# Optimization experiments

Hardware: AMD Instinct MI355X
Metric: run time of the kernel (lower is better)

## Reference

```python
import jax, jax.numpy as jnp
import numpy as np

N_NODES = 10000
N_EDGES = 160000
N_GRAPHS = 64
X_IN = 128
HID = 64
EDGE_DIM = 16
HEADS = 4
# (in_dim, out_dim_per_head) for the 3 TransformerConv layers (concat=False)
DIMS = [(X_IN, HID), (HID, 2 * HID), (2 * HID, HID)]
WNAMES = [f"{n}{l}" for l in (1, 2, 3) for n in ("wq", "bq", "wk", "bk", "wv", "bv", "we", "ws", "bs")]


def setup_inputs() -> dict:
    key = jax.random.key(0)
    ks = iter(jax.random.split(key, 64))
    inp = {}
    inp["x"] = jax.random.normal(next(ks), (N_NODES, X_IN), jnp.float32)
    inp["edge_index"] = jax.random.randint(next(ks), (2, N_EDGES), 0, N_NODES)
    inp["edge_attr"] = jax.random.normal(next(ks), (N_EDGES, EDGE_DIM), jnp.float32)
    inp["batch"] = jnp.sort(jax.random.randint(next(ks), (N_NODES,), 0, N_GRAPHS))
    for l, (din, dout) in enumerate(DIMS, 1):
        hd = HEADS * dout
        for nm, shape in [("wq", (din, hd)), ("wk", (din, hd)), ("wv", (din, hd)),
                          ("we", (EDGE_DIM, hd)), ("ws", (din, dout))]:
            inp[f"{nm}{l}"] = jax.random.normal(next(ks), shape, jnp.float32) * 0.05
        inp[f"bq{l}"] = jnp.zeros((hd,), jnp.float32)
        inp[f"bk{l}"] = jnp.zeros((hd,), jnp.float32)
        inp[f"bv{l}"] = jnp.zeros((hd,), jnp.float32)
        inp[f"bs{l}"] = jnp.zeros((dout,), jnp.float32)
    return inp


def _transformer_conv(x, src, dst, edge_attr, wq, bq, wk, bk, wv, bv, we, ws, bs, dout):
    """PyG TransformerConv, concat=False, root_weight=True, with edge features."""
    N = x.shape[0]
    q = (x @ wq + bq).reshape(N, HEADS, dout)
    k = (x @ wk + bk).reshape(N, HEADS, dout)
    v = (x @ wv + bv).reshape(N, HEADS, dout)
    e = (edge_attr @ we).reshape(-1, HEADS, dout)  # [E, H, C]
    k_j = k[src] + e                               # edge-conditioned keys
    alpha = jnp.einsum("ehd,ehd->eh", q[dst], k_j) * (1.0 / float(dout) ** 0.5)  # [E, H]
    # numerically stable segment softmax over incoming edges of each dst node
    a_max = jax.ops.segment_max(alpha, dst, num_segments=N)
    ex = jnp.exp(alpha - a_max[dst])
    den = jax.ops.segment_sum(ex, dst, num_segments=N)
    attn = ex / den[dst]
    agg = jax.ops.segment_sum((v[src] + e) * attn[..., None], dst, num_segments=N)  # [N, H, C]
    return agg.mean(axis=1) + x @ ws + bs  # concat=False -> head mean; + skip


def _forward(x, edge_attr, edge_index, batch, params):
    src, dst = edge_index[0], edge_index[1]
    h = x
    for l, (_, dout) in enumerate(DIMS, 1):
        p = [params[f"{n}{l}"] for n in ("wq", "bq", "wk", "bk", "wv", "bv", "we", "ws", "bs")]
        h = jax.nn.elu(_transformer_conv(h, src, dst, edge_attr, *p, dout))
    # global mean pool over graphs
    s = jax.ops.segment_sum(h, batch, num_segments=N_GRAPHS)
    cnt = jax.ops.segment_sum(jnp.ones((h.shape[0], 1), h.dtype), batch, num_segments=N_GRAPHS)
    return s / jnp.maximum(cnt, 1.0)


def reference(x, edge_index, edge_attr, batch,
              wq1, bq1, wk1, bk1, wv1, bv1, we1, ws1, bs1,
              wq2, bq2, wk2, bk2, wv2, bv2, we2, ws2, bs2,
              wq3, bq3, wk3, bk3, wv3, bv3, we3, ws3, bs3):
    params = dict(locals())
    return _forward(x, edge_attr, edge_index, batch, params)
```

## Files before the change

kernel.cpp:

```cpp
#include <hip/hip_runtime.h>
#include <hip/hip_fp16.h>
#include <math.h>

#define N_NODES 10000
#define N_EDGES 160000
#define N_GRAPHS 64

using half8 = __attribute__((ext_vector_type(8))) _Float16;
using floatx4 = __attribute__((ext_vector_type(4))) float;
using h2v = __attribute__((ext_vector_type(2))) _Float16;

template <int NV> struct KW;
template <> struct KW<1> { using T = uint2; };
template <> struct KW<2> { using T = uint4; };

__device__ inline void cvt_kv(const uint2& w, float4* dst) {
  float2 a = __half22float2(*reinterpret_cast<const __half2*>(&w.x));
  float2 b = __half22float2(*reinterpret_cast<const __half2*>(&w.y));
  dst[0] = make_float4(a.x, a.y, b.x, b.y);
}
__device__ inline void cvt_kv(const uint4& w, float4* dst) {
  float2 a = __half22float2(*reinterpret_cast<const __half2*>(&w.x));
  float2 b = __half22float2(*reinterpret_cast<const __half2*>(&w.y));
  float2 c = __half22float2(*reinterpret_cast<const __half2*>(&w.z));
  float2 d = __half22float2(*reinterpret_cast<const __half2*>(&w.w));
  dst[0] = make_float4(a.x, a.y, b.x, b.y);
  dst[1] = make_float4(c.x, c.y, d.x, d.y);
}

#if __has_builtin(__builtin_amdgcn_fdot2)
__device__ inline float dot_qk(const uint2& k, const uint2& q, float c) {
  c = __builtin_amdgcn_fdot2(__builtin_bit_cast(h2v, k.x), __builtin_bit_cast(h2v, q.x), c, false);
  c = __builtin_amdgcn_fdot2(__builtin_bit_cast(h2v, k.y), __builtin_bit_cast(h2v, q.y), c, false);
  return c;
}
__device__ inline float dot_qk(const uint4& k, const uint4& q, float c) {
  c = __builtin_amdgcn_fdot2(__builtin_bit_cast(h2v, k.x), __builtin_bit_cast(h2v, q.x), c, false);
  c = __builtin_amdgcn_fdot2(__builtin_bit_cast(h2v, k.y), __builtin_bit_cast(h2v, q.y), c, false);
  c = __builtin_amdgcn_fdot2(__builtin_bit_cast(h2v, k.z), __builtin_bit_cast(h2v, q.z), c, false);
  c = __builtin_amdgcn_fdot2(__builtin_bit_cast(h2v, k.w), __builtin_bit_cast(h2v, q.w), c, false);
  return c;
}
#else
__device__ inline float dot_qk(const uint2& k, const uint2& q, float c) {
  float4 kk[1], qq[1];
  cvt_kv(k, kk); cvt_kv(q, qq);
  return c + qq[0].x * kk[0].x + qq[0].y * kk[0].y + qq[0].z * kk[0].z + qq[0].w * kk[0].w;
}
__device__ inline float dot_qk(const uint4& k, const uint4& q, float c) {
  float4 kk[2], qq[2];
  cvt_kv(k, kk); cvt_kv(q, qq);
  c += qq[0].x * kk[0].x + qq[0].y * kk[0].y + qq[0].z * kk[0].z + qq[0].w * kk[0].w;
  c += qq[1].x * kk[1].x + qq[1].y * kk[1].y + qq[1].z * kk[1].z + qq[1].w * kk[1].w;
  return c;
}
#endif

template <int K, int HD, int DOUT>
__global__ __launch_bounds__(256) void gemm_mfma(
    const __half* __restrict__ A, const __half* __restrict__ Wp,
    const float* __restrict__ bias, __half* __restrict__ QS,
    __half* __restrict__ KV, int M) {
  constexpr int QSS = HD + 64 + DOUT;
  constexpr int KVS = 2 * HD;
  constexpr int KS = K / 32;
  constexpr int NV = DOUT / 64;
  __shared__ __half st[64][72];
  const int tid = threadIdx.x;
  const int wave = tid >> 6, lane = tid & 63;
  const int quad = lane >> 4, n16 = lane & 15;
  const int row0 = blockIdx.y * 64;
  const int col0 = blockIdx.x * 64;
  const int nblk0 = blockIdx.x * 4;

  const int arow = min(row0 + wave * 16 + n16, M - 1);
  half8 afrag[KS];
#pragma unroll
  for (int s = 0; s < KS; ++s)
    afrag[s] = *reinterpret_cast<const half8*>(A + (size_t)arow * K + s * 32 + quad * 8);

  floatx4 acc[4];
#pragma unroll
  for (int t = 0; t < 4; ++t) {
    acc[t] = (floatx4){0.f, 0.f, 0.f, 0.f};
#pragma unroll
    for (int s = 0; s < KS; ++s) {
      half8 bf = *reinterpret_cast<const half8*>(
          Wp + (((size_t)(nblk0 + t) * KS + s) * 64 + lane) * 8);
      acc[t] = __builtin_amdgcn_mfma_f32_16x16x32_f16(afrag[s], bf, acc[t], 0, 0, 0);
    }
  }

#pragma unroll
  for (int t = 0; t < 4; ++t) {
    float bv = bias[col0 + t * 16 + n16];
#pragma unroll
    for (int r = 0; r < 4; ++r)
      st[wave * 16 + quad * 4 + r][t * 16 + n16] = __float2half(acc[t][r] + bv);
  }
  __syncthreads();

  __half* dp;
  int colb, stride;
  bool kvreg = false;
  if (col0 < HD + 64) {
    dp = QS; colb = col0; stride = QSS;
  } else if (col0 < 3 * HD + 64) {
    dp = KV; colb = col0 - HD - 64; stride = KVS; kvreg = true;
  } else {
    dp = QS; colb = HD + 64 + (col0 - 3 * HD - 64); stride = QSS;
  }
  for (int c = tid; c < 512; c += 256) {
    int r = c >> 3, seg = c & 7;
    int row = row0 + r;
    if (row >= M) continue;
    if (NV == 1 && kvreg) {
      int dfull = colb + seg * 8;
      bool isK = dfull < HD;
      int dd = isK ? dfull : dfull - HD;
      int hh = dd >> 6, d0 = dd & 63;
      int o = hh * 128 + 2 * d0 + (isK ? 0 : 4);
      uint4 w = *reinterpret_cast<const uint4*>(&st[r][seg * 8]);
      *reinterpret_cast<uint2*>(dp + (size_t)row * stride + o) = make_uint2(w.x, w.y);
      *reinterpret_cast<uint2*>(dp + (size_t)row * stride + o + 8) = make_uint2(w.z, w.w);
    } else {
      *reinterpret_cast<uint4*>(dp + (size_t)row * stride + colb + seg * 8) =
          *reinterpret_cast<const uint4*>(&st[r][seg * 8]);
    }
  }
}

__device__ inline void pack_layer(int i, int K, int HD, int DOUT, float scale,
                                  const float* wq, const float* wk,
                                  const float* wv, const float* wsk,
                                  const float* we, const float* bq,
                                  const float* bk, const float* bv,
                                  const float* bs, __half* Wp, float* bcat) {
  const int W = 3 * HD + DOUT + 64;
  const int KS = K / 32;
  if (i < K * W) {
    int j = i & 7, lane = (i >> 3) & 63, fs = i >> 9;
    int nblk = fs / KS, s = fs - nblk * KS;
    int quad = lane >> 4, n = lane & 15;
    int k = s * 32 + quad * 8 + j, c = nblk * 16 + n;
    float v;
    if (c < HD) {
      v = wq[k * HD + c] * scale;
    } else if (c < HD + 64) {
      int gi = c - HD, hh = gi >> 4, d = gi & 15;
      float a = 0.f;
      for (int cc = 0; cc < DOUT; ++cc)
        a += wq[k * HD + hh * DOUT + cc] * we[d * HD + hh * DOUT + cc];
      v = a * scale;
    } else if (c < 2 * HD + 64) {
      v = wk[k * HD + (c - HD - 64)];
    } else if (c < 3 * HD + 64) {
      v = wv[k * HD + (c - 2 * HD - 64)];
    } else {
      v = wsk[k * DOUT + (c - 3 * HD - 64)];
    }
    Wp[i] = __float2half(v);
  } else {
    int c = i - K * W;
    float v;
    if (c < HD) {
      v = bq[c] * scale;
    } else if (c < HD + 64) {
      int gi = c - HD, hh = gi >> 4, d = gi & 15;
      float a = 0.f;
      for (int cc = 0; cc < DOUT; ++cc)
        a += bq[hh * DOUT + cc] * we[d * HD + hh * DOUT + cc];
      v = a * scale;
    } else if (c < 2 * HD + 64) {
      v = bk[c - HD - 64];
    } else if (c < 3 * HD + 64) {
      v = bv[c - 2 * HD - 64];
    } else {
      v = bs[c - 3 * HD - 64];
    }
    bcat[c] = v;
  }
}

#define T1 115584
#define T2 227904
#define T3 343488
#define TCONV (N_NODES * 32)
#define TTOT (T3 + TCONV)

__global__ void pack_all(
    const float* wq1, const float* wk1, const float* wv1, const float* ws1,
    const float* we1, const float* bq1, const float* bk1, const float* bv1,
    const float* bs1,
    const float* wq2, const float* wk2, const float* wv2, const float* ws2,
    const float* we2, const float* bq2, const float* bk2, const float* bv2,
    const float* bs2,
    const float* wq3, const float* wk3, const float* wv3, const float* ws3,
    const float* we3, const float* bq3, const float* bk3, const float* bv3,
    const float* bs3,
    __half* W1, float* b1, __half* W2, float* b2, __half* W3, float* b3,
    const float* x, __half* x16) {
  const float SC1 = 0.125f, SC2 = 0.08838834764831845f;
  for (int i = blockIdx.x * blockDim.x + threadIdx.x; i < TTOT;
       i += gridDim.x * blockDim.x) {
    if (i < T1)
      pack_layer(i, 128, 256, 64, SC1, wq1, wk1, wv1, ws1, we1, bq1, bk1, bv1, bs1, W1, b1);
    else if (i < T2)
      pack_layer(i - T1, 64, 512, 128, SC2, wq2, wk2, wv2, ws2, we2, bq2, bk2, bv2, bs2, W2, b2);
    else if (i < T3)
      pack_layer(i - T2, 128, 256, 64, SC1, wq3, wk3, wv3, ws3, we3, bq3, bk3, bv3, bs3, W3, b3);
    else {
      int k = i - T3;
      float4 v = reinterpret_cast<const float4*>(x)[k];
      __half2* o = reinterpret_cast<__half2*>(x16) + 2 * k;
      o[0] = __floats2half2_rn(v.x, v.y);
      o[1] = __floats2half2_rn(v.z, v.w);
    }
  }
}

__global__ void count_dst(const int* __restrict__ dst, int* __restrict__ cnt) {
  int e = blockIdx.x * blockDim.x + threadIdx.x;
  if (e < N_EDGES) atomicAdd(&cnt[dst[e]], 1);
}

__global__ __launch_bounds__(1024) void scan_offs(const int* __restrict__ cnt,
                                                  int* __restrict__ offs,
                                                  int* __restrict__ perm) {
  __shared__ int part[1024];
  __shared__ int hist[256], hstart[256], hcur[256];
  const int t = threadIdx.x;
  const int chunk = (N_NODES + 1023) / 1024;
  const int b = t * chunk;
  const int e = min(N_NODES, b + chunk);
  if (t < 256) { hist[t] = 0; hcur[t] = 0; }
  __syncthreads();
  int s = 0;
  for (int i = b; i < e; ++i) {
    int d = cnt[i];
    s += d;
    atomicAdd(&hist[min(d, 255)], 1);
  }
  part[t] = s;
  __syncthreads();
  for (int off = 1; off < 1024; off <<= 1) {
    int v = (t >= off) ? part[t - off] : 0;
    __syncthreads();
    part[t] += v;
    __syncthreads();
  }
  if (t == 0) {
    int acc = 0;
    for (int bk = 255; bk >= 0; --bk) { hstart[bk] = acc; acc += hist[bk]; }
    offs[N_NODES] = part[1023];
  }
  __syncthreads();
  int pre = (t == 0) ? 0 : part[t - 1];
  for (int i = b; i < e; ++i) {
    offs[i] = pre;
    int d = cnt[i];
    pre += d;
    int bkt = min(d, 255);
    int pos = hstart[bkt] + atomicAdd(&hcur[bkt], 1);
    perm[pos] = i;
  }
}

__global__ void scatter_csr(const int* __restrict__ src, const int* __restrict__ dst,
                            const float* __restrict__ edge_attr,
                            const int* __restrict__ offs, int* __restrict__ cursor,
                            int* __restrict__ csr_src, float* __restrict__ csr_ea) {
  int e = blockIdx.x * blockDim.x + threadIdx.x;
  if (e < N_EDGES) {
    int d = dst[e];
    int pos = offs[d] + atomicAdd(&cursor[d], 1);
    csr_src[pos] = src[e];
    float4* o4 = reinterpret_cast<float4*>(csr_ea + (size_t)pos * 16);
    const float4* s4 = reinterpret_cast<const float4*>(edge_attr + (size_t)e * 16);
    o4[0] = s4[0]; o4[1] = s4[1]; o4[2] = s4[2]; o4[3] = s4[3];
  }
}

template <int DOUT, bool W32>
__global__ __launch_bounds__(128) void edge_attn(
    const __half* __restrict__ QS, const __half* __restrict__ KV,
    const float* __restrict__ we, const int* __restrict__ csr_src,
    const float* __restrict__ csr_ea, const int* __restrict__ offs,
    const int* __restrict__ perm, float* __restrict__ out,
    __half* __restrict__ out16) {
  constexpr int HD = 4 * DOUT;
  constexpr int QSS = HD + 64 + DOUT;
  constexpr int KVS = 2 * HD;
  constexpr int NV = DOUT / 64;
  using KWT = typename KW<NV>::T;

  const int lane = threadIdx.x & 63;
  const int h = lane >> 4, t16 = lane & 15;
  const int n = perm[blockIdx.x * 2 + (threadIdx.x >> 6)];
  const int c0 = t16 * 4 * NV;
  const int kvoff = h * 128 + t16 * 8;

  const __half* base = QS + (size_t)n * QSS;
  KWT qw = *reinterpret_cast<const KWT*>(base + h * DOUT + c0);
  float4 acc[NV];
#pragma unroll
  for (int v = 0; v < NV; ++v) acc[v] = make_float4(0.f, 0.f, 0.f, 0.f);
  const float g = __half2float(base[HD + h * 16 + t16]);

  float lsum = 0.f, tacc = 0.f;

  const int s0 = offs[n], s1 = offs[n + 1];

  float eaA[4], eaB[4], eaC[4];
  uint4 krA[4], vrA[4], krB[4], vrB[4], krC[4], vrC[4];

  for (int cb = s0; cb < s1; cb += 64) {
    const int m = min(64, s1 - cb);
    const int idx = csr_src[cb + min(lane, m - 1)];
    const int ng = m >> 2;

    auto load_grp = [&](int gb, float (&ea)[4], uint4 (&kr)[4], uint4 (&vr)[4]) {
      const int bi = cb + gb;
#pragma unroll
      for (int j = 0; j < 4; ++j) ea[j] = csr_ea[(size_t)(bi + j) * 16 + t16];
#pragma unroll
      for (int j = 0; j < 4; ++j) {
        int sj = __shfl(idx, gb + j);
        const __half* rb = KV + (size_t)sj * KVS + kvoff;
        kr[j] = *reinterpret_cast<const uint4*>(rb);
        if (NV == 2) vr[j] = *reinterpret_cast<const uint4*>(rb + HD);
      }
    };

    auto compute_grp = [&](float (&ea)[4], uint4 (&kr)[4], uint4 (&vr)[4]) {
      float a[4];
#pragma unroll
      for (int j = 0; j < 4; ++j) {
        if (NV == 1)
          a[j] = dot_qk(make_uint2(kr[j].x, kr[j].y),
                        *reinterpret_cast<const uint2*>(&qw), ea[j] * g);
        else
          a[j] = dot_qk(*reinterpret_cast<const uint4*>(&kr[j]),
                        *reinterpret_cast<const uint4*>(&qw), ea[j] * g);
      }
#pragma unroll
      for (int j = 0; j < 4; ++j) {
        a[j] += __shfl_xor(a[j], 1);
        a[j] += __shfl_xor(a[j], 2);
        a[j] += __shfl_xor(a[j], 4);
        a[j] += __shfl_xor(a[j], 8);
      }
      float p0 = __expf(a[0]), p1 = __expf(a[1]);
      float p2 = __expf(a[2]), p3 = __expf(a[3]);
      lsum += p0 + p1 + p2 + p3;
      tacc += p0 * ea[0] + p1 * ea[1] + p2 * ea[2] + p3 * ea[3];
      float pj[4] = {p0, p1, p2, p3};
#pragma unroll
      for (int j = 0; j < 4; ++j) {
        float4 vv[NV];
        if (NV == 1)
          cvt_kv(make_uint2(kr[j].z, kr[j].w), vv);
        else
          cvt_kv(vr[j], vv);
#pragma unroll
        for (int v = 0; v < NV; ++v) {
          acc[v].x += pj[j] * vv[v].x;
          acc[v].y += pj[j] * vv[v].y;
          acc[v].z += pj[j] * vv[v].z;
          acc[v].w += pj[j] * vv[v].w;
        }
      }
    };

    if (ng) {
      load_grp(0, eaA, krA, vrA);
      if (ng > 1) load_grp(4, eaB, krB, vrB);
      int gi = 0;
      for (;;) {
        if (gi + 2 < ng) load_grp((gi + 2) * 4, eaC, krC, vrC);
        compute_grp(eaA, krA, vrA);
        if (++gi >= ng) break;
        if (gi + 2 < ng) load_grp((gi + 2) * 4, eaA, krA, vrA);
        compute_grp(eaB, krB, vrB);
        if (++gi >= ng) break;
        if (gi + 2 < ng) load_grp((gi + 2) * 4, eaB, krB, vrB);
        compute_grp(eaC, krC, vrC);
        if (++gi >= ng) break;
      }
    }

    for (int e = ng * 4; e < m; ++e) {
      int sj = __shfl(idx, e);
      float ea0 = csr_ea[(size_t)(cb + e) * 16 + t16];
      const __half* rb = KV + (size_t)sj * KVS + kvoff;
      uint4 kw = *reinterpret_cast<const uint4*>(rb);
      float a;
      float4 vv[NV];
      if (NV == 1) {
        a = dot_qk(make_uint2(kw.x, kw.y),
                   *reinterpret_cast<const uint2*>(&qw), ea0 * g);
        cvt_kv(make_uint2(kw.z, kw.w), vv);
      } else {
        uint4 vw = *reinterpret_cast<const uint4*>(rb + HD);
        a = dot_qk(kw, *reinterpret_cast<const uint4*>(&qw), ea0 * g);
        cvt_kv(vw, vv);
      }
      a += __shfl_xor(a, 1);
      a += __shfl_xor(a, 2);
      a += __shfl_xor(a, 4);
      a += __shfl_xor(a, 8);
      float p = __expf(a);
      lsum += p;
      tacc += p * ea0;
#pragma unroll
      for (int v = 0; v < NV; ++v) {
        acc[v].x += p * vv[v].x;
        acc[v].y += p * vv[v].y;
        acc[v].z += p * vv[v].z;
        acc[v].w += p * vv[v].w;
      }
    }
  }

  float invl = (lsum > 0.f) ? 1.f / lsum : 0.f;
  float tn = tacc * invl;
  float4 val[NV];
#pragma unroll
  for (int v = 0; v < NV; ++v) {
    val[v].x = acc[v].x * invl; val[v].y = acc[v].y * invl;
    val[v].z = acc[v].z * invl; val[v].w = acc[v].w * invl;
  }
#pragma unroll
  for (int d = 0; d < 16; ++d) {
    float td = __shfl(tn, (lane & 48) | d);
    const float* wb = we + d * HD + h * DOUT + c0;
#pragma unroll
    for (int v = 0; v < NV; ++v) {
      float4 w4 = *reinterpret_cast<const float4*>(wb + 4 * v);
      val[v].x += td * w4.x; val[v].y += td * w4.y;
      val[v].z += td * w4.z; val[v].w += td * w4.w;
    }
  }
#pragma unroll
  for (int v = 0; v < NV; ++v) {
    val[v].x += __shfl_xor(val[v].x, 16); val[v].x += __shfl_xor(val[v].x, 32);
    val[v].y += __shfl_xor(val[v].y, 16); val[v].y += __shfl_xor(val[v].y, 32);
    val[v].z += __shfl_xor(val[v].z, 16); val[v].z += __shfl_xor(val[v].z, 32);
    val[v].w += __shfl_xor(val[v].w, 16); val[v].w += __shfl_xor(val[v].w, 32);
  }
  if (h == 0) {
    KWT sw = *reinterpret_cast<const KWT*>(base + HD + 64 + c0);
    float4 sk[NV];
    cvt_kv(sw, sk);
#pragma unroll
    for (int v = 0; v < NV; ++v) {
      float4 o;
      o.x = 0.25f * val[v].x + sk[v].x;
      o.y = 0.25f * val[v].y + sk[v].y;
      o.z = 0.25f * val[v].z + sk[v].z;
      o.w = 0.25f * val[v].w + sk[v].w;
      o.x = (o.x > 0.f) ? o.x : expm1f(o.x);
      o.y = (o.y > 0.f) ? o.y : expm1f(o.y);
      o.z = (o.z > 0.f) ? o.z : expm1f(o.z);
      o.w = (o.w > 0.f) ? o.w : expm1f(o.w);
      if (W32)
        *reinterpret_cast<float4*>(out + (size_t)n * DOUT + c0 + 4 * v) = o;
      __half2* o16 = reinterpret_cast<__half2*>(out16 + (size_t)n * DOUT + c0 + 4 * v);
      o16[0] = __floats2half2_rn(o.x, o.y);
      o16[1] = __floats2half2_rn(o.z, o.w);
    }
  }
}

__device__ inline int lower_bound(const int* b, int n, int v) {
  int lo = 0, hi = n;
  while (lo < hi) {
    int mid = (lo + hi) >> 1;
    if (b[mid] < v) lo = mid + 1; else hi = mid;
  }
  return lo;
}

__global__ __launch_bounds__(256) void pool_all(const float* __restrict__ h,
                                                const int* __restrict__ batch,
                                                float* __restrict__ out) {
  const int g = blockIdx.x;
  const int start = lower_bound(batch, N_NODES, g);
  const int end = lower_bound(batch, N_NODES, g + 1);
  const int c = threadIdx.x & 63, j = threadIdx.x >> 6;
  float s = 0.f;
  for (int n = start + j; n < end; n += 4) s += h[(size_t)n * 64 + c];
  __shared__ float red[4][64];
  red[j][c] = s;
  __syncthreads();
  if (j == 0) {
    float tot = red[0][c] + red[1][c] + red[2][c] + red[3][c];
    out[g * 64 + c] = tot / (float)max(end - start, 1);
  }
}

extern "C" void kernel_launch(void* const* d_in, const int* in_sizes, int n_in,
                              void* d_out, int out_size, void* d_ws, size_t ws_size,
                              hipStream_t stream) {
  const float* x = (const float*)d_in[0];
  const int* edge_index = (const int*)d_in[1];
  const float* edge_attr = (const float*)d_in[2];
  const int* batch = (const int*)d_in[3];
  const int* srcp = edge_index;
  const int* dstp = edge_index + N_EDGES;

  const bool dict_order = in_sizes[5] > 1024;
  const float *wq[3], *wk[3], *wv[3], *wep[3], *wsk[3], *bq[3], *bk[3], *bv[3], *bs[3];
  for (int L = 0; L < 3; ++L) {
    int b = 4 + L * 9;
    if (dict_order) {
      wq[L] = (const float*)d_in[b + 0];
      wk[L] = (const float*)d_in[b + 1];
      wv[L] = (const float*)d_in[b + 2];
      wep[L] = (const float*)d_in[b + 3];
      wsk[L] = (const float*)d_in[b + 4];
      bq[L] = (const float*)d_in[b + 5];
      bk[L] = (const float*)d_in[b + 6];
      bv[L] = (const float*)d_in[b + 7];
      bs[L] = (const float*)d_in[b + 8];
    } else {
      wq[L] = (const float*)d_in[b + 0];
      bq[L] = (const float*)d_in[b + 1];
      wk[L] = (const float*)d_in[b + 2];
      bk[L] = (const float*)d_in[b + 3];
      wv[L] = (const float*)d_in[b + 4];
      bv[L] = (const float*)d_in[b + 5];
      wep[L] = (const float*)d_in[b + 6];
      wsk[L] = (const float*)d_in[b + 7];
      bs[L] = (const float*)d_in[b + 8];
    }
  }

  char* p = (char*)d_ws;
  __half* qs = (__half*)p;    p += (size_t)N_NODES * 704 * 2;
  __half* kv = (__half*)p;    p += (size_t)N_NODES * 1024 * 2;
  float* h1 = (float*)p;      p += (size_t)N_NODES * 64 * 4;
  __half* x16 = (__half*)p;   p += (size_t)N_NODES * 128 * 2;
  __half* h16 = (__half*)p;   p += (size_t)N_NODES * 128 * 2;
  __half* W1 = (__half*)p;    p += 128 * 896 * 2;
  __half* W2 = (__half*)p;    p += 64 * 1728 * 2;
  __half* W3 = (__half*)p;    p += 128 * 896 * 2;
  float* b1 = (float*)p;      p += 896 * 4;
  float* b2 = (float*)p;      p += 1728 * 4;
  float* b3 = (float*)p;      p += 896 * 4;
  float* csr_ea = (float*)p;  p += (size_t)N_EDGES * 16 * 4;
  int* cnt = (int*)p;         p += N_NODES * 4;
  int* cursor = (int*)p;      p += N_NODES * 4;
  int* offs = (int*)p;        p += (N_NODES + 1) * 4;
  int* perm = (int*)p;        p += N_NODES * 4;
  int* csr_src = (int*)p;     p += N_EDGES * 4;

  pack_all<<<1024, 256, 0, stream>>>(
      wq[0], wk[0], wv[0], wsk[0], wep[0], bq[0], bk[0], bv[0], bs[0],
      wq[1], wk[1], wv[1], wsk[1], wep[1], bq[1], bk[1], bv[1], bs[1],
      wq[2], wk[2], wv[2], wsk[2], wep[2], bq[2], bk[2], bv[2], bs[2],
      W1, b1, W2, b2, W3, b3, x, x16);

  hipMemsetAsync(cnt, 0, 2 * N_NODES * sizeof(int), stream);
  count_dst<<<(N_EDGES + 255) / 256, 256, 0, stream>>>(dstp, cnt);
  scan_offs<<<1, 1024, 0, stream>>>(cnt, offs, perm);
  scatter_csr<<<(N_EDGES + 255) / 256, 256, 0, stream>>>(srcp, dstp, edge_attr,
                                                         offs, cursor, csr_src, csr_ea);

  const int MT = (N_NODES + 63) / 64;
  gemm_mfma<128, 256, 64><<<dim3(896 / 64, MT), 256, 0, stream>>>(x16, W1, b1, qs,
                                                                  kv, N_NODES);
  edge_attn<64, false><<<N_NODES / 2, 128, 0, stream>>>(qs, kv, wep[0], csr_src,
                                                        csr_ea, offs, perm, h1, h16);
  gemm_mfma<64, 512, 128><<<dim3(1728 / 64, MT), 256, 0, stream>>>(h16, W2, b2, qs,
                                                                   kv, N_NODES);
  edge_attn<128, false><<<N_NODES / 2, 128, 0, stream>>>(qs, kv, wep[1], csr_src,
                                                         csr_ea, offs, perm, h1, h16);
  gemm_mfma<128, 256, 64><<<dim3(896 / 64, MT), 256, 0, stream>>>(h16, W3, b3, qs,
                                                                  kv, N_NODES);
  edge_attn<64, true><<<N_NODES / 2, 128, 0, stream>>>(qs, kv, wep[2], csr_src,
                                                       csr_ea, offs, perm, h1, x16);

  pool_all<<<N_GRAPHS, 256, 0, stream>>>(h1, batch, (float*)d_out);
}
```

Baseline: 329.0 us.

## Fuse global mean pool into last attention layer via atomics

Drops the separate pool_all kernel. The last edge_attn layer now atomically adds its ELU outputs, prescaled by per-graph inverse counts that scan_offs computes, straight into the output. The memset of the counters and output is folded into pack_all, removing one launch and the h1 fp32 write/read round trip. It also adds an occupancy hint of 3 to edge_attn launch bounds. The cost is 640k float atomics on 64x64 output addresses, with heavy contention because batch is sorted and neighbouring nodes share a graph.

```diff
diff --git a/kernel.cpp b/kernel.cpp
--- a/kernel.cpp
+++ b/kernel.cpp
@@ -55,6 +55,15 @@
   return c;
 }
 #endif
+
+__device__ inline int lower_bound(const int* b, int n, int v) {
+  int lo = 0, hi = n;
+  while (lo < hi) {
+    int mid = (lo + hi) >> 1;
+    if (b[mid] < v) lo = mid + 1; else hi = mid;
+  }
+  return lo;
+}
 
 template <int K, int HD, int DOUT>
 __global__ __launch_bounds__(256) void gemm_mfma(
@@ -187,6 +196,7 @@
 #define T3 343488
 #define TCONV (N_NODES * 32)
 #define TTOT (T3 + TCONV)
+#define NZERO (2 * N_NODES + N_GRAPHS * 64)
 
 __global__ void pack_all(
     const float* wq1, const float* wk1, const float* wv1, const float* ws1,
@@ -199,8 +209,13 @@
     const float* we3, const float* bq3, const float* bk3, const float* bv3,
     const float* bs3,
     __half* W1, float* b1, __half* W2, float* b2, __half* W3, float* b3,
-    const float* x, __half* x16) {
+    const float* x, __half* x16, int* cntz, float* doutz) {
   const float SC1 = 0.125f, SC2 = 0.08838834764831845f;
+  for (int i = blockIdx.x * blockDim.x + threadIdx.x; i < NZERO;
+       i += gridDim.x * blockDim.x) {
+    if (i < 2 * N_NODES) cntz[i] = 0;
+    else doutz[i - 2 * N_NODES] = 0.f;
+  }
   for (int i = blockIdx.x * blockDim.x + threadIdx.x; i < TTOT;
        i += gridDim.x * blockDim.x) {
     if (i < T1)
@@ -226,10 +241,17 @@
 
 __global__ __launch_bounds__(1024) void scan_offs(const int* __restrict__ cnt,
                                                   int* __restrict__ offs,
-                                                  int* __restrict__ perm) {
+                                                  int* __restrict__ perm,
+                                                  const int* __restrict__ batch,
+                                                  float* __restrict__ invc) {
   __shared__ int part[1024];
   __shared__ int hist[256], hstart[256], hcur[256];
   const int t = threadIdx.x;
+  if (t < N_GRAPHS) {
+    int st = lower_bound(batch, N_NODES, t);
+    int en = lower_bound(batch, N_NODES, t + 1);
+    invc[t] = 1.f / (float)max(en - st, 1);
+  }
   const int chunk = (N_NODES + 1023) / 1024;
   const int b = t * chunk;
   const int e = min(N_NODES, b + chunk);
@@ -281,12 +303,13 @@
   }
 }
 
-template <int DOUT, bool W32>
-__global__ __launch_bounds__(128) void edge_attn(
+template <int DOUT, bool POOL>
+__global__ __launch_bounds__(128, 3) void edge_attn(
     const __half* __restrict__ QS, const __half* __restrict__ KV,
     const float* __restrict__ we, const int* __restrict__ csr_src,
     const float* __restrict__ csr_ea, const int* __restrict__ offs,
-    const int* __restrict__ perm, float* __restrict__ out,
+    const int* __restrict__ perm, const int* __restrict__ batch,
+    const float* __restrict__ invc, float* __restrict__ out,
     __half* __restrict__ out16) {
   constexpr int HD = 4 * DOUT;
   constexpr int QSS = HD + 64 + DOUT;
@@ -452,6 +475,13 @@
     KWT sw = *reinterpret_cast<const KWT*>(base + HD + 64 + c0);
     float4 sk[NV];
     cvt_kv(sw, sk);
+    float pinv;
+    float* gb;
+    if (POOL) {
+      int gg = batch[n];
+      pinv = invc[gg];
+      gb = out + gg * 64;
+    }
 #pragma unroll
     for (int v = 0; v < NV; ++v) {
       float4 o;
@@ -463,39 +493,18 @@
       o.y = (o.y > 0.f) ? o.y : expm1f(o.y);
       o.z = (o.z > 0.f) ? o.z : expm1f(o.z);
       o.w = (o.w > 0.f) ? o.w : expm1f(o.w);
-      if (W32)
-        *reinterpret_cast<float4*>(out + (size_t)n * DOUT + c0 + 4 * v) = o;
-      __half2* o16 = reinterpret_cast<__half2*>(out16 + (size_t)n * DOUT + c0 + 4 * v);
-      o16[0] = __floats2half2_rn(o.x, o.y);
-      o16[1] = __floats2half2_rn(o.z, o.w);
-    }
-  }
-}
-
-__device__ inline int lower_bound(const int* b, int n, int v) {
-  int lo = 0, hi = n;
-  while (lo < hi) {
-    int mid = (lo + hi) >> 1;
-    if (b[mid] < v) lo = mid + 1; else hi = mid;
-  }
-  return lo;
-}
-
-__global__ __launch_bounds__(256) void pool_all(const float* __restrict__ h,
-                                                const int* __restrict__ batch,
-                                                float* __restrict__ out) {
-  const int g = blockIdx.x;
-  const int start = lower_bound(batch, N_NODES, g);
-  const int end = lower_bound(batch, N_NODES, g + 1);
-  const int c = threadIdx.x & 63, j = threadIdx.x >> 6;
-  float s = 0.f;
-  for (int n = start + j; n < end; n += 4) s += h[(size_t)n * 64 + c];
-  __shared__ float red[4][64];
-  red[j][c] = s;
-  __syncthreads();
-  if (j == 0) {
-    float tot = red[0][c] + red[1][c] + red[2][c] + red[3][c];
-    out[g * 64 + c] = tot / (float)max(end - start, 1);
+      if (POOL) {
+        float* op = gb + c0 + 4 * v;
+        atomicAdd(op + 0, o.x * pinv);
+        atomicAdd(op + 1, o.y * pinv);
+        atomicAdd(op + 2, o.z * pinv);
+        atomicAdd(op + 3, o.w * pinv);
+      } else {
+        __half2* o16 = reinterpret_cast<__half2*>(out16 + (size_t)n * DOUT + c0 + 4 * v);
+        o16[0] = __floats2half2_rn(o.x, o.y);
+        o16[1] = __floats2half2_rn(o.z, o.w);
+      }
+    }
   }
 }
 
@@ -548,6 +557,7 @@
   float* b1 = (float*)p;      p += 896 * 4;
   float* b2 = (float*)p;      p += 1728 * 4;
   float* b3 = (float*)p;      p += 896 * 4;
+  float* invc = (float*)p;    p += 64 * 4;
   float* csr_ea = (float*)p;  p += (size_t)N_EDGES * 16 * 4;
   int* cnt = (int*)p;         p += N_NODES * 4;
   int* cursor = (int*)p;      p += N_NODES * 4;
@@ -559,27 +569,24 @@
       wq[0], wk[0], wv[0], wsk[0], wep[0], bq[0], bk[0], bv[0], bs[0],
       wq[1], wk[1], wv[1], wsk[1], wep[1], bq[1], bk[1], bv[1], bs[1],
       wq[2], wk[2], wv[2], wsk[2], wep[2], bq[2], bk[2], bv[2], bs[2],
-      W1, b1, W2, b2, W3, b3, x, x16);
-
-  hipMemsetAsync(cnt, 0, 2 * N_NODES * sizeof(int), stream);
+      W1, b1, W2, b2, W3, b3, x, x16, cnt, (float*)d_out);
+
   count_dst<<<(N_EDGES + 255) / 256, 256, 0, stream>>>(dstp, cnt);
-  scan_offs<<<1, 1024, 0, stream>>>(cnt, offs, perm);
+  scan_offs<<<1, 1024, 0, stream>>>(cnt, offs, perm, batch, invc);
   scatter_csr<<<(N_EDGES + 255) / 256, 256, 0, stream>>>(srcp, dstp, edge_attr,
                                                          offs, cursor, csr_src, csr_ea);
 
   const int MT = (N_NODES + 63) / 64;
   gemm_mfma<128, 256, 64><<<dim3(896 / 64, MT), 256, 0, stream>>>(x16, W1, b1, qs,
                                                                   kv, N_NODES);
-  edge_attn<64, false><<<N_NODES / 2, 128, 0, stream>>>(qs, kv, wep[0], csr_src,
-                                                        csr_ea, offs, perm, h1, h16);
+  edge_attn<64, false><<<N_NODES / 2, 128, 0, stream>>>(
+      qs, kv, wep[0], csr_src, csr_ea, offs, perm, batch, invc, h1, h16);
   gemm_mfma<64, 512, 128><<<dim3(1728 / 64, MT), 256, 0, stream>>>(h16, W2, b2, qs,
                                                                    kv, N_NODES);
-  edge_attn<128, false><<<N_NODES / 2, 128, 0, stream>>>(qs, kv, wep[1], csr_src,
-                                                         csr_ea, offs, perm, h1, h16);
+  edge_attn<128, false><<<N_NODES / 2, 128, 0, stream>>>(
+      qs, kv, wep[1], csr_src, csr_ea, offs, perm, batch, invc, h1, h16);
   gemm_mfma<128, 256, 64><<<dim3(896 / 64, MT), 256, 0, stream>>>(h16, W3, b3, qs,
                                                                   kv, N_NODES);
-  edge_attn<64, true><<<N_NODES / 2, 128, 0, stream>>>(qs, kv, wep[2], csr_src,
-                                                       csr_ea, offs, perm, h1, x16);
-
-  pool_all<<<N_GRAPHS, 256, 0, stream>>>(h1, batch, (float*)d_out);
-}
+  edge_attn<64, true><<<N_NODES / 2, 128, 0, stream>>>(
+      qs, kv, wep[2], csr_src, csr_ea, offs, perm, batch, invc, (float*)d_out, x16);
+}
```

Result: no change. 325.3 us (-1.1%).
